# Kernel optimization log

Hardware: AMD Instinct MI355X
Metric: run time of the kernel (lower is better)

Reference implementation:

```python
import jax, jax.numpy as jnp
import numpy as np

NUM_USERS = 100000
NUM_ITEMS = 50000
EMBED = 64
S_NNZ = NUM_USERS * 32   # avg social degree 32
R_NNZ = NUM_USERS * 50   # avg 50 rated items per user
BATCH = 8192


def setup_inputs() -> dict:
    key = jax.random.key(0)
    ks = jax.random.split(key, 12)
    d = EMBED
    # Embedding tables (xavier-uniform style scale)
    U = jax.random.uniform(ks[0], (NUM_USERS, d), jnp.float32, -1.0, 1.0) * np.sqrt(6.0 / (NUM_USERS + d))
    V = jax.random.uniform(ks[1], (NUM_ITEMS, d), jnp.float32, -1.0, 1.0) * np.sqrt(6.0 / (NUM_ITEMS + d))
    # Diffusion layer weights: Linear(2d -> d). Stored as [2d, d] (x @ W + b).
    lim = np.sqrt(6.0 / (3 * d))
    W0 = jax.random.uniform(ks[2], (2 * d, d), jnp.float32, -lim, lim)
    b0 = jnp.zeros((d,), jnp.float32)
    W1 = jax.random.uniform(ks[3], (2 * d, d), jnp.float32, -lim, lim)
    b1 = jnp.zeros((d,), jnp.float32)
    # Sparse social matrix S [NUM_USERS, NUM_USERS], COO edge lists, row-normalized values.
    S_row = jax.random.randint(ks[4], (S_NNZ,), 0, NUM_USERS, jnp.int32)
    S_col = jax.random.randint(ks[5], (S_NNZ,), 0, NUM_USERS, jnp.int32)
    S_val = jnp.full((S_NNZ,), 1.0 / 32.0, jnp.float32)
    # Sparse rating matrix R [NUM_USERS, NUM_ITEMS]
    R_row = jax.random.randint(ks[6], (R_NNZ,), 0, NUM_USERS, jnp.int32)
    R_col = jax.random.randint(ks[7], (R_NNZ,), 0, NUM_ITEMS, jnp.int32)
    R_val = jnp.full((R_NNZ,), 1.0 / 50.0, jnp.float32)
    batch_user = jax.random.randint(ks[8], (BATCH,), 0, NUM_USERS, jnp.int64 if jax.config.jax_enable_x64 else jnp.int32)
    batch_pos_item = jax.random.randint(ks[9], (BATCH,), 0, NUM_ITEMS, jnp.int32)
    batch_neg_item = jax.random.randint(ks[10], (BATCH,), 0, NUM_ITEMS, jnp.int32)
    return dict(batch_user=batch_user, batch_pos_item=batch_pos_item, batch_neg_item=batch_neg_item,
                U=U, V=V, W0=W0, b0=b0, W1=W1, b1=b1,
                S_row=S_row, S_col=S_col, S_val=S_val,
                R_row=R_row, R_col=R_col, R_val=R_val)


def _spmm(row, col, val, X, n_rows):
    # (sparse [n_rows, n] COO) @ X : gather + scale + segment-sum
    return jax.ops.segment_sum(val[:, None] * X[col], row, num_segments=n_rows)


def reference(batch_user, batch_pos_item, batch_neg_item, U, V, W0, b0, W1, b1,
              S_row, S_col, S_val, R_row, R_col, R_val):
    # Diffusion layers: U <- relu(concat([S @ U, U]) @ W + b)
    for W, b in ((W0, b0), (W1, b1)):
        agg = _spmm(S_row, S_col, S_val, U, NUM_USERS)          # [num_users, d]
        U = jax.nn.relu(jnp.concatenate([agg, U], axis=1) @ W + b)
    user_g = U + _spmm(R_row, R_col, R_val, V, NUM_USERS)        # [num_users, d]
    bu = user_g[batch_user]          # [B, d]
    bp = V[batch_pos_item]           # [B, d]
    bn = V[batch_neg_item]           # [B, d]
    return (bu, bp, bn)
```

## Files before the change

kernel.cpp:

```cpp
#include <hip/hip_runtime.h>
#include <hip/hip_bf16.h>

#define NUM_USERS 100000
#define NUM_ITEMS 50000
#define EMBED     64
#define S_NNZ     (NUM_USERS * 32)
#define R_NNZ     (NUM_USERS * 50)
#define BATCH     8192

#define NB    512
#define NCH   1024
#define CHUNK (S_NNZ / NCH)
#define BROWS 196

#define SEGCAP 160


__global__ __launch_bounds__(256) void k_p1hist(const int* __restrict__ rows, int* __restrict__ cnt_t,
                                                int* __restrict__ head, unsigned* __restrict__ bitmap,
                                                int* __restrict__ cntR) {
    __shared__ int h[NB];
    int t = threadIdx.x, b = blockIdx.x;
    int gid = b * 256 + t;
    for (int i = gid; i < NUM_USERS; i += NCH * 256) head[i] = -1;
    for (int i = gid; i < (NUM_USERS + 31) / 32; i += NCH * 256) bitmap[i] = 0;
    for (int i = gid; i < BATCH; i += NCH * 256) cntR[i] = 0;
    for (int i = t; i < NB; i += 256) h[i] = 0;
    __syncthreads();
    int base = b * CHUNK;
    for (int i = t; i < CHUNK; i += 256) atomicAdd(&h[rows[base + i] / BROWS], 1);
    __syncthreads();
    for (int i = t; i < NB; i += 256) cnt_t[i * NCH + b] = h[i];
}

__global__ __launch_bounds__(1024) void k_scan1(const int* __restrict__ cnt, int* __restrict__ excl,
                                                int* __restrict__ bsums, int n,
                                                const int* __restrict__ bu, int* __restrict__ head,
                                                int* __restrict__ nxt, unsigned* __restrict__ bitmap) {
    int t = threadIdx.x;
    int i = blockIdx.x * 1024 + t;
    if (i < BATCH) {
        int u = bu[i];
        nxt[i] = atomicExch(&head[u], i);
        atomicOr(&bitmap[u >> 5], 1u << (u & 31));
    }
    __shared__ int buf[1024];
    int x = (i < n) ? cnt[i] : 0;
    buf[t] = x;
    __syncthreads();
    for (int off = 1; off < 1024; off <<= 1) {
        int y = (t >= off) ? buf[t - off] : 0;
        __syncthreads();
        buf[t] += y;
        __syncthreads();
    }
    if (i < n) excl[i] = buf[t] - x;
    if (t == 1023) bsums[blockIdx.x] = buf[1023];
}

__global__ __launch_bounds__(1024) void k_scan2(int* __restrict__ bsums, int nb, int* __restrict__ total_slot) {
    __shared__ int buf[1024];
    int t = threadIdx.x;
    int x = (t < nb) ? bsums[t] : 0;
    buf[t] = x;
    __syncthreads();
    for (int off = 1; off < 1024; off <<= 1) {
        int y = (t >= off) ? buf[t - off] : 0;
        __syncthreads();
        buf[t] += y;
        __syncthreads();
    }
    if (t < nb) bsums[t] = buf[t] - x;
    if (t == 1023) total_slot[0] = buf[1023];
}

__global__ void k_scan3b(int* __restrict__ a, const int* __restrict__ bsums, int n) {
    int i = blockIdx.x * blockDim.x + threadIdx.x;
    if (i < n) a[i] += bsums[i >> 10];
}

__global__ __launch_bounds__(256) void k_p1scatter(const int* __restrict__ rows, const int* __restrict__ cols,
                                                   const float* __restrict__ vals, const int* __restrict__ cnt_t,
                                                   int2* __restrict__ tmpE,
                                                   const float* __restrict__ U, __hip_bfloat16* __restrict__ U16) {
    __shared__ int cur[NB];
    int t = threadIdx.x, b = blockIdx.x;
    for (int i = t; i < NB; i += 256) cur[i] = cnt_t[i * NCH + b];
    __syncthreads();
    int base = b * CHUNK;
    for (int i = t; i < CHUNK; i += 256) {
        int e  = base + i;
        int r  = rows[e];
        int bk = r / BROWS;
        int pos = atomicAdd(&cur[bk], 1);
        tmpE[pos] = make_int2(((r - bk * BROWS) << 17) | cols[e], __float_as_int(vals[e]));
    }
    const int total = NUM_USERS * EMBED;
    for (int i = b * 256 + t; i < total; i += NCH * 256) U16[i] = __float2bfloat16(U[i]);
}

__global__ __launch_bounds__(512) void k_p2(const int2* __restrict__ tmpE, const int* __restrict__ cnt_t,
                                            int* __restrict__ rowptr, int2* __restrict__ colval) {
    __shared__ int h[512];
    __shared__ int s[512];
    __shared__ int cur[512];
    int t = threadIdx.x, k = blockIdx.x;
    int beg = cnt_t[k * NCH];
    int end = (k < NB - 1) ? cnt_t[(k + 1) * NCH] : S_NNZ;
    h[t] = 0;
    __syncthreads();
    for (int j = beg + t; j < end; j += 512) atomicAdd(&h[((unsigned)tmpE[j].x) >> 17], 1);
    __syncthreads();
    s[t] = h[t];
    __syncthreads();
    for (int off = 1; off < 512; off <<= 1) {
        int y = (t >= off) ? s[t - off] : 0;
        __syncthreads();
        s[t] += y;
        __syncthreads();
    }
    int excl = s[t] - h[t];
    int gr   = k * BROWS + t;
    if (t <= BROWS && gr <= NUM_USERS) rowptr[gr] = beg + excl;
    cur[t] = beg + excl;
    __syncthreads();
    for (int j = beg + t; j < end; j += 512) {
        int2 e  = tmpE[j];
        int pos = atomicAdd(&cur[((unsigned)e.x) >> 17], 1);
        colval[pos] = make_int2(e.x & 0x1FFFF, e.y);
    }
}

__global__ __launch_bounds__(256) void k_spmm16p(const int* __restrict__ rowptr,
                                                 const int2* __restrict__ colval,
                                                 const __hip_bfloat16* __restrict__ X,
                                                 float* __restrict__ Y, int n_pairs) {
    int w    = blockIdx.x * (blockDim.x >> 6) + (threadIdx.x >> 6);
    int lane = threadIdx.x & 63;
    if (w >= n_pairs) return;
    int r0   = 2 * w;
    int beg0 = rowptr[r0], mid = rowptr[r0 + 1], end1 = rowptr[r0 + 2];
    float acc0 = 0.0f, acc1 = 0.0f;
    int j0 = beg0, j1 = mid;
    int jend0 = beg0 + ((mid - beg0) & ~7);
    int jend1 = mid + ((end1 - mid) & ~7);
    while (j0 < jend0 && j1 < jend1) {
        int2 ca[8], cb[8];
#pragma unroll
        for (int u = 0; u < 8; ++u) ca[u] = colval[j0 + u];
#pragma unroll
        for (int u = 0; u < 8; ++u) cb[u] = colval[j1 + u];
        float xa[8], xb[8];
#pragma unroll
        for (int u = 0; u < 8; ++u) xa[u] = __bfloat162float(X[(size_t)ca[u].x * EMBED + lane]);
#pragma unroll
        for (int u = 0; u < 8; ++u) xb[u] = __bfloat162float(X[(size_t)cb[u].x * EMBED + lane]);
#pragma unroll
        for (int u = 0; u < 8; ++u) acc0 = fmaf(__int_as_float(ca[u].y), xa[u], acc0);
#pragma unroll
        for (int u = 0; u < 8; ++u) acc1 = fmaf(__int_as_float(cb[u].y), xb[u], acc1);
        j0 += 8; j1 += 8;
    }
    for (; j0 < jend0; j0 += 8) {
        int2 cv[8];
#pragma unroll
        for (int u = 0; u < 8; ++u) cv[u] = colval[j0 + u];
        float x[8];
#pragma unroll
        for (int u = 0; u < 8; ++u) x[u] = __bfloat162float(X[(size_t)cv[u].x * EMBED + lane]);
#pragma unroll
        for (int u = 0; u < 8; ++u) acc0 = fmaf(__int_as_float(cv[u].y), x[u], acc0);
    }
    for (; j1 < jend1; j1 += 8) {
        int2 cv[8];
#pragma unroll
        for (int u = 0; u < 8; ++u) cv[u] = colval[j1 + u];
        float x[8];
#pragma unroll
        for (int u = 0; u < 8; ++u) x[u] = __bfloat162float(X[(size_t)cv[u].x * EMBED + lane]);
#pragma unroll
        for (int u = 0; u < 8; ++u) acc1 = fmaf(__int_as_float(cv[u].y), x[u], acc1);
    }
    for (; j0 < mid; ++j0)
        acc0 = fmaf(__int_as_float(colval[j0].y), __bfloat162float(X[(size_t)colval[j0].x * EMBED + lane]), acc0);
    for (; j1 < end1; ++j1)
        acc1 = fmaf(__int_as_float(colval[j1].y), __bfloat162float(X[(size_t)colval[j1].x * EMBED + lane]), acc1);
    Y[(size_t)r0 * EMBED + lane]       = acc0;
    Y[(size_t)(r0 + 1) * EMBED + lane] = acc1;
}

__global__ __launch_bounds__(256) void k_spmm_batch16(const int* __restrict__ rowptr,
                                                      const int2* __restrict__ colval,
                                                      const __hip_bfloat16* __restrict__ X,
                                                      const int* __restrict__ bu,
                                                      float* __restrict__ Agg2, int n) {
    int w    = blockIdx.x * (blockDim.x >> 6) + (threadIdx.x >> 6);
    int lane = threadIdx.x & 63;
    if (w >= n) return;
    int r   = bu[w];
    int beg = rowptr[r], end = rowptr[r + 1];
    float acc = 0.0f;
    int j    = beg;
    int jend = beg + ((end - beg) & ~7);
    for (; j < jend; j += 8) {
        int2 cv[8];
#pragma unroll
        for (int u = 0; u < 8; ++u) cv[u] = colval[j + u];
        float x[8];
#pragma unroll
        for (int u = 0; u < 8; ++u) x[u] = __bfloat162float(X[(size_t)cv[u].x * EMBED + lane]);
#pragma unroll
        for (int u = 0; u < 8; ++u) acc = fmaf(__int_as_float(cv[u].y), x[u], acc);
    }
    for (; j < end; ++j)
        acc = fmaf(__int_as_float(colval[j].y), __bfloat162float(X[(size_t)colval[j].x * EMBED + lane]), acc);
    Agg2[(size_t)w * EMBED + lane] = acc;
}


__global__ __launch_bounds__(256) void k_layer(const float* __restrict__ Agg,
                                               const float* __restrict__ Uin,
                                               float* __restrict__ Uout,
                                               __hip_bfloat16* __restrict__ Uout16,
                                               const float* __restrict__ W,
                                               const float* __restrict__ b) {
    __shared__ __align__(16) float Wt[64 * 128];
    int t = threadIdx.x;
    for (int i = t; i < 128 * 64; i += 256) {
        int k = i >> 6, c = i & 63;
        Wt[c * 128 + ((((k >> 2) ^ (c & 7)) << 2) | (k & 3))] = W[i];
    }
    int rl = __builtin_amdgcn_readfirstlane(t >> 6);
    int c  = t & 63;
    int rbase = blockIdx.x * 16 + rl * 4;
    __syncthreads();
    const float4* Wt4 = (const float4*)Wt;
    int  csw   = c & 7;
    int  cbase = c * 32;
    const float4* a0 = (const float4*)(Agg + (size_t)(rbase + 0) * EMBED);
    const float4* a1 = (const float4*)(Agg + (size_t)(rbase + 1) * EMBED);
    const float4* a2 = (const float4*)(Agg + (size_t)(rbase + 2) * EMBED);
    const float4* a3 = (const float4*)(Agg + (size_t)(rbase + 3) * EMBED);
    const float4* u0 = (const float4*)(Uin + (size_t)(rbase + 0) * EMBED);
    const float4* u1 = (const float4*)(Uin + (size_t)(rbase + 1) * EMBED);
    const float4* u2 = (const float4*)(Uin + (size_t)(rbase + 2) * EMBED);
    const float4* u3 = (const float4*)(Uin + (size_t)(rbase + 3) * EMBED);
    float bias = b[c];
    float acc0 = bias, acc1 = bias, acc2 = bias, acc3 = bias;
#pragma unroll 4
    for (int k4 = 0; k4 < 16; ++k4) {
        float4 w4 = Wt4[cbase + (k4 ^ csw)];
        float4 x0 = a0[k4], x1 = a1[k4], x2 = a2[k4], x3 = a3[k4];
        acc0 = fmaf(x0.x, w4.x, acc0); acc0 = fmaf(x0.y, w4.y, acc0); acc0 = fmaf(x0.z, w4.z, acc0); acc0 = fmaf(x0.w, w4.w, acc0);
        acc1 = fmaf(x1.x, w4.x, acc1); acc1 = fmaf(x1.y, w4.y, acc1); acc1 = fmaf(x1.z, w4.z, acc1); acc1 = fmaf(x1.w, w4.w, acc1);
        acc2 = fmaf(x2.x, w4.x, acc2); acc2 = fmaf(x2.y, w4.y, acc2); acc2 = fmaf(x2.z, w4.z, acc2); acc2 = fmaf(x2.w, w4.w, acc2);
        acc3 = fmaf(x3.x, w4.x, acc3); acc3 = fmaf(x3.y, w4.y, acc3); acc3 = fmaf(x3.z, w4.z, acc3); acc3 = fmaf(x3.w, w4.w, acc3);
    }
#pragma unroll 4
    for (int k4 = 16; k4 < 32; ++k4) {
        float4 w4 = Wt4[cbase + (k4 ^ csw)];
        float4 x0 = u0[k4 - 16], x1 = u1[k4 - 16], x2 = u2[k4 - 16], x3 = u3[k4 - 16];
        acc0 = fmaf(x0.x, w4.x, acc0); acc0 = fmaf(x0.y, w4.y, acc0); acc0 = fmaf(x0.z, w4.z, acc0); acc0 = fmaf(x0.w, w4.w, acc0);
        acc1 = fmaf(x1.x, w4.x, acc1); acc1 = fmaf(x1.y, w4.y, acc1); acc1 = fmaf(x1.z, w4.z, acc1); acc1 = fmaf(x1.w, w4.w, acc1);
        acc2 = fmaf(x2.x, w4.x, acc2); acc2 = fmaf(x2.y, w4.y, acc2); acc2 = fmaf(x2.z, w4.z, acc2); acc2 = fmaf(x2.w, w4.w, acc2);
        acc3 = fmaf(x3.x, w4.x, acc3); acc3 = fmaf(x3.y, w4.y, acc3); acc3 = fmaf(x3.z, w4.z, acc3); acc3 = fmaf(x3.w, w4.w, acc3);
    }
    float v0 = fmaxf(acc0, 0.0f), v1 = fmaxf(acc1, 0.0f), v2 = fmaxf(acc2, 0.0f), v3 = fmaxf(acc3, 0.0f);
    Uout[(size_t)(rbase + 0) * EMBED + c] = v0;
    Uout[(size_t)(rbase + 1) * EMBED + c] = v1;
    Uout[(size_t)(rbase + 2) * EMBED + c] = v2;
    Uout[(size_t)(rbase + 3) * EMBED + c] = v3;
    Uout16[(size_t)(rbase + 0) * EMBED + c] = __float2bfloat16(v0);
    Uout16[(size_t)(rbase + 1) * EMBED + c] = __float2bfloat16(v1);
    Uout16[(size_t)(rbase + 2) * EMBED + c] = __float2bfloat16(v2);
    Uout16[(size_t)(rbase + 3) * EMBED + c] = __float2bfloat16(v3);
}

__global__ __launch_bounds__(256) void k_layer_batch(const float* __restrict__ Agg2,
                                                     const float* __restrict__ Uin,
                                                     const int* __restrict__ bu,
                                                     float* __restrict__ out0,
                                                     const float* __restrict__ W,
                                                     const float* __restrict__ b,
                                                     const float* __restrict__ V,
                                                     const int* __restrict__ bp,
                                                     const int* __restrict__ bn) {
    __shared__ __align__(16) float Wt[64 * 128];
    int t = threadIdx.x;
    for (int i = t; i < 128 * 64; i += 256) {
        int k = i >> 6, c = i & 63;
        Wt[c * 128 + ((((k >> 2) ^ (c & 7)) << 2) | (k & 3))] = W[i];
    }
    int rl = __builtin_amdgcn_readfirstlane(t >> 6);
    int c  = t & 63;
    int sbase = blockIdx.x * 16 + rl * 4;
    int r0 = bu[sbase + 0], r1 = bu[sbase + 1], r2 = bu[sbase + 2], r3 = bu[sbase + 3];
    __syncthreads();
    const float4* Wt4 = (const float4*)Wt;
    int  csw   = c & 7;
    int  cbase = c * 32;
    const float4* a0 = (const float4*)(Agg2 + (size_t)(sbase + 0) * EMBED);
    const float4* a1 = (const float4*)(Agg2 + (size_t)(sbase + 1) * EMBED);
    const float4* a2 = (const float4*)(Agg2 + (size_t)(sbase + 2) * EMBED);
    const float4* a3 = (const float4*)(Agg2 + (size_t)(sbase + 3) * EMBED);
    const float4* u0 = (const float4*)(Uin + (size_t)r0 * EMBED);
    const float4* u1 = (const float4*)(Uin + (size_t)r1 * EMBED);
    const float4* u2 = (const float4*)(Uin + (size_t)r2 * EMBED);
    const float4* u3 = (const float4*)(Uin + (size_t)r3 * EMBED);
    float bias = b[c];
    float acc0 = bias, acc1 = bias, acc2 = bias, acc3 = bias;
#pragma unroll 4
    for (int k4 = 0; k4 < 16; ++k4) {
        float4 w4 = Wt4[cbase + (k4 ^ csw)];
        float4 x0 = a0[k4], x1 = a1[k4], x2 = a2[k4], x3 = a3[k4];
        acc0 = fmaf(x0.x, w4.x, acc0); acc0 = fmaf(x0.y, w4.y, acc0); acc0 = fmaf(x0.z, w4.z, acc0); acc0 = fmaf(x0.w, w4.w, acc0);
        acc1 = fmaf(x1.x, w4.x, acc1); acc1 = fmaf(x1.y, w4.y, acc1); acc1 = fmaf(x1.z, w4.z, acc1); acc1 = fmaf(x1.w, w4.w, acc1);
        acc2 = fmaf(x2.x, w4.x, acc2); acc2 = fmaf(x2.y, w4.y, acc2); acc2 = fmaf(x2.z, w4.z, acc2); acc2 = fmaf(x2.w, w4.w, acc2);
        acc3 = fmaf(x3.x, w4.x, acc3); acc3 = fmaf(x3.y, w4.y, acc3); acc3 = fmaf(x3.z, w4.z, acc3); acc3 = fmaf(x3.w, w4.w, acc3);
    }
#pragma unroll 4
    for (int k4 = 16; k4 < 32; ++k4) {
        float4 w4 = Wt4[cbase + (k4 ^ csw)];
        float4 x0 = u0[k4 - 16], x1 = u1[k4 - 16], x2 = u2[k4 - 16], x3 = u3[k4 - 16];
        acc0 = fmaf(x0.x, w4.x, acc0); acc0 = fmaf(x0.y, w4.y, acc0); acc0 = fmaf(x0.z, w4.z, acc0); acc0 = fmaf(x0.w, w4.w, acc0);
        acc1 = fmaf(x1.x, w4.x, acc1); acc1 = fmaf(x1.y, w4.y, acc1); acc1 = fmaf(x1.z, w4.z, acc1); acc1 = fmaf(x1.w, w4.w, acc1);
        acc2 = fmaf(x2.x, w4.x, acc2); acc2 = fmaf(x2.y, w4.y, acc2); acc2 = fmaf(x2.z, w4.z, acc2); acc2 = fmaf(x2.w, w4.w, acc2);
        acc3 = fmaf(x3.x, w4.x, acc3); acc3 = fmaf(x3.y, w4.y, acc3); acc3 = fmaf(x3.z, w4.z, acc3); acc3 = fmaf(x3.w, w4.w, acc3);
    }
    out0[(size_t)(sbase + 0) * EMBED + c] = fmaxf(acc0, 0.0f);
    out0[(size_t)(sbase + 1) * EMBED + c] = fmaxf(acc1, 0.0f);
    out0[(size_t)(sbase + 2) * EMBED + c] = fmaxf(acc2, 0.0f);
    out0[(size_t)(sbase + 3) * EMBED + c] = fmaxf(acc3, 0.0f);
#pragma unroll
    for (int q = 0; q < 4; ++q) {
        int s = sbase + q;
        out0[(size_t)(BATCH + s) * EMBED + c]     = V[(size_t)bp[s] * EMBED + c];
        out0[(size_t)(2 * BATCH + s) * EMBED + c] = V[(size_t)bn[s] * EMBED + c];
    }
}


__global__ __launch_bounds__(256) void k_rseg(const int* __restrict__ rows,
                                              const int* __restrict__ cols,
                                              const float* __restrict__ vals,
                                              const unsigned* __restrict__ bitmap,
                                              const int* __restrict__ head,
                                              int* __restrict__ cntR,
                                              int2* __restrict__ seg, int nnz,
                                              const float* __restrict__ V,
                                              __hip_bfloat16* __restrict__ V16) {
    int e = blockIdx.x * blockDim.x + threadIdx.x;
    if (e < NUM_ITEMS * EMBED) V16[e] = __float2bfloat16(V[e]);
    if (e >= nnz) return;
    int r = rows[e];
    if (!((bitmap[(unsigned)r >> 5] >> (r & 31)) & 1u)) return;
    int s   = head[r];
    int pos = atomicAdd(&cntR[s], 1);
    if (pos < SEGCAP) seg[s * SEGCAP + pos] = make_int2(cols[e], __float_as_int(vals[e]));
}

__global__ __launch_bounds__(256) void k_rspmm(const int* __restrict__ cntR,
                                               const int2* __restrict__ seg,
                                               const __hip_bfloat16* __restrict__ V16,
                                               const int* __restrict__ bu,
                                               const int* __restrict__ head,
                                               const int* __restrict__ nxt,
                                               float* __restrict__ out0) {
    int s    = blockIdx.x * (blockDim.x >> 6) + (threadIdx.x >> 6);
    int lane = threadIdx.x & 63;
    if (s >= BATCH) return;
    if (head[bu[s]] != s) return;
    int n = cntR[s];
    if (n > SEGCAP) n = SEGCAP;
    const int2* cv2 = seg + (size_t)s * SEGCAP;
    float acc = 0.0f;
    int j    = 0;
    int jend = n & ~7;
    for (; j < jend; j += 8) {
        int2 cv[8];
#pragma unroll
        for (int u = 0; u < 8; ++u) cv[u] = cv2[j + u];
        float x[8];
#pragma unroll
        for (int u = 0; u < 8; ++u) x[u] = __bfloat162float(V16[(size_t)cv[u].x * EMBED + lane]);
#pragma unroll
        for (int u = 0; u < 8; ++u) acc = fmaf(__int_as_float(cv[u].y), x[u], acc);
    }
    for (; j < n; ++j)
        acc = fmaf(__int_as_float(cv2[j].y), __bfloat162float(V16[(size_t)cv2[j].x * EMBED + lane]), acc);
    int slot = s;
    while (slot >= 0) {
        out0[(size_t)slot * EMBED + lane] += acc;
        slot = nxt[slot];
    }
}


extern "C" void kernel_launch(void* const* d_in, const int* in_sizes, int n_in,
                              void* d_out, int out_size, void* d_ws, size_t ws_size,
                              hipStream_t stream) {
    const int*   batch_user = (const int*)d_in[0];
    const int*   batch_pos  = (const int*)d_in[1];
    const int*   batch_neg  = (const int*)d_in[2];
    const float* U     = (const float*)d_in[3];
    const float* V     = (const float*)d_in[4];
    const float* W0    = (const float*)d_in[5];
    const float* b0    = (const float*)d_in[6];
    const float* W1    = (const float*)d_in[7];
    const float* b1    = (const float*)d_in[8];
    const int*   S_row = (const int*)d_in[9];
    const int*   S_col = (const int*)d_in[10];
    const float* S_val = (const float*)d_in[11];
    const int*   R_row = (const int*)d_in[12];
    const int*   R_col = (const int*)d_in[13];
    const float* R_val = (const float*)d_in[14];
    float* out = (float*)d_out;

    const size_t tabElems = (size_t)NUM_USERS * EMBED;

    char* wsb = (char*)d_ws;
    size_t o = 0;
    float* A       = (float*)(wsb + o); o += tabElems * 4;
    float* B       = (float*)(wsb + o); o += tabElems * 4;
    float* Agg2    = (float*)(wsb + o); o += (size_t)BATCH * EMBED * 4;
    int*   rowptrS = (int*)(wsb + o);   o += (NUM_USERS + 1) * 4;
    int*   cnt_t   = (int*)(wsb + o);   o += (size_t)NB * NCH * 4;
    int*   bsums   = (int*)(wsb + o);   o += 1024 * 4;
    int*   head    = (int*)(wsb + o);   o += NUM_USERS * 4;
    int*   nxt     = (int*)(wsb + o);   o += BATCH * 4;
    int*   cntR    = (int*)(wsb + o);   o += BATCH * 4;
    unsigned* bitmap = (unsigned*)(wsb + o); o += ((NUM_USERS + 31) / 32) * 4;
    o = (o + 7) & ~(size_t)7;
    int2*  colvalS = (int2*)(wsb + o);  o += (size_t)S_NNZ * 8;
    __hip_bfloat16* X16 = (__hip_bfloat16*)(wsb + o); o += tabElems * 2;

    int2* tmpE = (int2*)A;
    int2* seg  = (int2*)B;

    const int pair_blocks  = (NUM_USERS / 2) / 4;
    const int layer_blocks = (NUM_USERS + 15) / 16;

    k_p1hist<<<NCH, 256, 0, stream>>>(S_row, cnt_t, head, bitmap, cntR);
    k_scan1<<<(NB * NCH) / 1024, 1024, 0, stream>>>(cnt_t, cnt_t, bsums, NB * NCH,
                                                    batch_user, head, nxt, bitmap);
    k_scan2<<<1, 1024, 0, stream>>>(bsums, (NB * NCH) / 1024, &bsums[512]);
    k_scan3b<<<(NB * NCH) / 256, 256, 0, stream>>>(cnt_t, bsums, NB * NCH);
    k_p1scatter<<<NCH, 256, 0, stream>>>(S_row, S_col, S_val, cnt_t, tmpE, U, X16);
    k_p2<<<NB, 512, 0, stream>>>(tmpE, cnt_t, rowptrS, colvalS);

    k_spmm16p<<<pair_blocks, 256, 0, stream>>>(rowptrS, colvalS, X16, B, NUM_USERS / 2);
    k_layer<<<layer_blocks, 256, 0, stream>>>(B, U, A, X16, W0, b0);

    k_spmm_batch16<<<(BATCH * 64 + 255) / 256, 256, 0, stream>>>(rowptrS, colvalS, X16, batch_user, Agg2, BATCH);
    k_layer_batch<<<(BATCH + 15) / 16, 256, 0, stream>>>(Agg2, A, batch_user, out, W1, b1,
                                                         V, batch_pos, batch_neg);

    k_rseg<<<(R_NNZ + 255) / 256, 256, 0, stream>>>(R_row, R_col, R_val, bitmap, head, cntR, seg, R_NNZ,
                                                    V, X16);
    k_rspmm<<<(BATCH * 64 + 255) / 256, 256, 0, stream>>>(cntR, seg, X16, batch_user, head, nxt, out);
}
```

Before: 514.1 us.

## Fuse CSR build pipeline into one cooperative kernel with grid syncs

Six separate launches (histogram, three-stage scan, scatter, per-bucket sort) are merged into one cooperative kernel of 1024 blocks, with grid.sync() between phases. The scan is rewritten so each block covers 512 counts and block 0 scans the 1024 block sums. The aim is to remove launch gaps and the tiny single-block scan kernels. In exchange it pays five grid-wide barriers, and the bucket phase now uses 256 threads per bucket instead of 512, with half the blocks idle.

```diff
diff --git a/kernel.cpp b/kernel.cpp
--- a/kernel.cpp
+++ b/kernel.cpp
@@ -1,5 +1,8 @@
 #include <hip/hip_runtime.h>
 #include <hip/hip_bf16.h>
+#include <hip/hip_cooperative_groups.h>
+
+namespace cg = cooperative_groups;
 
 #define NUM_USERS 100000
 #define NUM_ITEMS 50000
@@ -16,118 +19,132 @@
 #define SEGCAP 160
 
 
-__global__ __launch_bounds__(256) void k_p1hist(const int* __restrict__ rows, int* __restrict__ cnt_t,
-                                                int* __restrict__ head, unsigned* __restrict__ bitmap,
-                                                int* __restrict__ cntR) {
-    __shared__ int h[NB];
+__global__ __launch_bounds__(256) void k_build(const int* __restrict__ rows,
+                                               const int* __restrict__ cols,
+                                               const float* __restrict__ vals,
+                                               int* __restrict__ cnt_t,
+                                               int* __restrict__ head,
+                                               unsigned* __restrict__ bitmap,
+                                               int* __restrict__ cntR,
+                                               const int* __restrict__ bu,
+                                               int* __restrict__ nxt,
+                                               int2* __restrict__ tmpE,
+                                               const float* __restrict__ U,
+                                               __hip_bfloat16* __restrict__ U16,
+                                               int* __restrict__ rowptr,
+                                               int2* __restrict__ colval,
+                                               int* __restrict__ bsums) {
+    cg::grid_group grid = cg::this_grid();
+    __shared__ int sh[768];
     int t = threadIdx.x, b = blockIdx.x;
-    int gid = b * 256 + t;
-    for (int i = gid; i < NUM_USERS; i += NCH * 256) head[i] = -1;
-    for (int i = gid; i < (NUM_USERS + 31) / 32; i += NCH * 256) bitmap[i] = 0;
-    for (int i = gid; i < BATCH; i += NCH * 256) cntR[i] = 0;
-    for (int i = t; i < NB; i += 256) h[i] = 0;
+    int base = b * CHUNK;
+
+    for (int i = b * 256 + t; i < NUM_USERS; i += NCH * 256) head[i] = -1;
+    for (int i = b * 256 + t; i < (NUM_USERS + 31) / 32; i += NCH * 256) bitmap[i] = 0;
+    for (int i = b * 256 + t; i < BATCH; i += NCH * 256) cntR[i] = 0;
+    for (int i = t; i < NB; i += 256) sh[i] = 0;
     __syncthreads();
-    int base = b * CHUNK;
-    for (int i = t; i < CHUNK; i += 256) atomicAdd(&h[rows[base + i] / BROWS], 1);
+    for (int i = t; i < CHUNK; i += 256) atomicAdd(&sh[rows[base + i] / BROWS], 1);
     __syncthreads();
-    for (int i = t; i < NB; i += 256) cnt_t[i * NCH + b] = h[i];
-}
-
-__global__ __launch_bounds__(1024) void k_scan1(const int* __restrict__ cnt, int* __restrict__ excl,
-                                                int* __restrict__ bsums, int n,
-                                                const int* __restrict__ bu, int* __restrict__ head,
-                                                int* __restrict__ nxt, unsigned* __restrict__ bitmap) {
-    int t = threadIdx.x;
-    int i = blockIdx.x * 1024 + t;
-    if (i < BATCH) {
-        int u = bu[i];
-        nxt[i] = atomicExch(&head[u], i);
-        atomicOr(&bitmap[u >> 5], 1u << (u & 31));
-    }
-    __shared__ int buf[1024];
-    int x = (i < n) ? cnt[i] : 0;
-    buf[t] = x;
-    __syncthreads();
-    for (int off = 1; off < 1024; off <<= 1) {
-        int y = (t >= off) ? buf[t - off] : 0;
-        __syncthreads();
-        buf[t] += y;
-        __syncthreads();
-    }
-    if (i < n) excl[i] = buf[t] - x;
-    if (t == 1023) bsums[blockIdx.x] = buf[1023];
-}
-
-__global__ __launch_bounds__(1024) void k_scan2(int* __restrict__ bsums, int nb, int* __restrict__ total_slot) {
-    __shared__ int buf[1024];
-    int t = threadIdx.x;
-    int x = (t < nb) ? bsums[t] : 0;
-    buf[t] = x;
-    __syncthreads();
-    for (int off = 1; off < 1024; off <<= 1) {
-        int y = (t >= off) ? buf[t - off] : 0;
-        __syncthreads();
-        buf[t] += y;
-        __syncthreads();
-    }
-    if (t < nb) bsums[t] = buf[t] - x;
-    if (t == 1023) total_slot[0] = buf[1023];
-}
-
-__global__ void k_scan3b(int* __restrict__ a, const int* __restrict__ bsums, int n) {
-    int i = blockIdx.x * blockDim.x + threadIdx.x;
-    if (i < n) a[i] += bsums[i >> 10];
-}
-
-__global__ __launch_bounds__(256) void k_p1scatter(const int* __restrict__ rows, const int* __restrict__ cols,
-                                                   const float* __restrict__ vals, const int* __restrict__ cnt_t,
-                                                   int2* __restrict__ tmpE,
-                                                   const float* __restrict__ U, __hip_bfloat16* __restrict__ U16) {
-    __shared__ int cur[NB];
-    int t = threadIdx.x, b = blockIdx.x;
-    for (int i = t; i < NB; i += 256) cur[i] = cnt_t[i * NCH + b];
-    __syncthreads();
-    int base = b * CHUNK;
-    for (int i = t; i < CHUNK; i += 256) {
-        int e  = base + i;
-        int r  = rows[e];
-        int bk = r / BROWS;
-        int pos = atomicAdd(&cur[bk], 1);
-        tmpE[pos] = make_int2(((r - bk * BROWS) << 17) | cols[e], __float_as_int(vals[e]));
-    }
-    const int total = NUM_USERS * EMBED;
-    for (int i = b * 256 + t; i < total; i += NCH * 256) U16[i] = __float2bfloat16(U[i]);
-}
-
-__global__ __launch_bounds__(512) void k_p2(const int2* __restrict__ tmpE, const int* __restrict__ cnt_t,
-                                            int* __restrict__ rowptr, int2* __restrict__ colval) {
-    __shared__ int h[512];
-    __shared__ int s[512];
-    __shared__ int cur[512];
-    int t = threadIdx.x, k = blockIdx.x;
-    int beg = cnt_t[k * NCH];
-    int end = (k < NB - 1) ? cnt_t[(k + 1) * NCH] : S_NNZ;
-    h[t] = 0;
-    __syncthreads();
-    for (int j = beg + t; j < end; j += 512) atomicAdd(&h[((unsigned)tmpE[j].x) >> 17], 1);
-    __syncthreads();
-    s[t] = h[t];
-    __syncthreads();
-    for (int off = 1; off < 512; off <<= 1) {
-        int y = (t >= off) ? s[t - off] : 0;
-        __syncthreads();
-        s[t] += y;
-        __syncthreads();
-    }
-    int excl = s[t] - h[t];
-    int gr   = k * BROWS + t;
-    if (t <= BROWS && gr <= NUM_USERS) rowptr[gr] = beg + excl;
-    cur[t] = beg + excl;
-    __syncthreads();
-    for (int j = beg + t; j < end; j += 512) {
-        int2 e  = tmpE[j];
-        int pos = atomicAdd(&cur[((unsigned)e.x) >> 17], 1);
-        colval[pos] = make_int2(e.x & 0x1FFFF, e.y);
+    for (int i = t; i < NB; i += 256) cnt_t[i * NCH + b] = sh[i];
+    grid.sync();
+
+    {
+        int i = b * 256 + t;
+        if (i < BATCH) {
+            int u = bu[i];
+            nxt[i] = atomicExch(&head[u], i);
+            atomicOr(&bitmap[u >> 5], 1u << (u & 31));
+        }
+        int i0 = b * 512 + 2 * t;
+        int x0 = cnt_t[i0], x1 = cnt_t[i0 + 1];
+        int s2 = x0 + x1;
+        sh[t] = s2;
+        __syncthreads();
+        for (int off = 1; off < 256; off <<= 1) {
+            int y = (t >= off) ? sh[t - off] : 0;
+            __syncthreads();
+            sh[t] += y;
+            __syncthreads();
+        }
+        int excl = sh[t] - s2;
+        cnt_t[i0]     = excl;
+        cnt_t[i0 + 1] = excl + x0;
+        if (t == 255) bsums[b] = sh[255];
+    }
+    grid.sync();
+
+    if (b == 0) {
+        int l0 = bsums[4 * t], l1 = bsums[4 * t + 1], l2 = bsums[4 * t + 2], l3 = bsums[4 * t + 3];
+        int s4 = l0 + l1 + l2 + l3;
+        sh[t] = s4;
+        __syncthreads();
+        for (int off = 1; off < 256; off <<= 1) {
+            int y = (t >= off) ? sh[t - off] : 0;
+            __syncthreads();
+            sh[t] += y;
+            __syncthreads();
+        }
+        int excl = sh[t] - s4;
+        bsums[4 * t]     = excl;
+        bsums[4 * t + 1] = excl + l0;
+        bsums[4 * t + 2] = excl + l0 + l1;
+        bsums[4 * t + 3] = excl + l0 + l1 + l2;
+    }
+    grid.sync();
+
+    {
+        int off = bsums[b];
+        int i0  = b * 512 + 2 * t;
+        cnt_t[i0]     += off;
+        cnt_t[i0 + 1] += off;
+    }
+    grid.sync();
+
+    {
+        for (int i = t; i < NB; i += 256) sh[i] = cnt_t[i * NCH + b];
+        __syncthreads();
+        for (int i = t; i < CHUNK; i += 256) {
+            int e  = base + i;
+            int r  = rows[e];
+            int bk = r / BROWS;
+            int pos = atomicAdd(&sh[bk], 1);
+            tmpE[pos] = make_int2(((r - bk * BROWS) << 17) | cols[e], __float_as_int(vals[e]));
+        }
+        const int total = NUM_USERS * EMBED;
+        for (int i = b * 256 + t; i < total; i += NCH * 256) U16[i] = __float2bfloat16(U[i]);
+    }
+    grid.sync();
+
+    if (b < NB) {
+        int k   = b;
+        int beg = cnt_t[k * NCH];
+        int end = (k < NB - 1) ? cnt_t[(k + 1) * NCH] : S_NNZ;
+        int* h2 = sh;
+        int* s2 = sh + 256;
+        int* cu = sh + 512;
+        h2[t] = 0;
+        __syncthreads();
+        for (int j = beg + t; j < end; j += 256) atomicAdd(&h2[((unsigned)tmpE[j].x) >> 17], 1);
+        __syncthreads();
+        s2[t] = h2[t];
+        __syncthreads();
+        for (int off = 1; off < 256; off <<= 1) {
+            int y = (t >= off) ? s2[t - off] : 0;
+            __syncthreads();
+            s2[t] += y;
+            __syncthreads();
+        }
+        int excl = s2[t] - h2[t];
+        int gr   = k * BROWS + t;
+        if (t <= BROWS && gr <= NUM_USERS) rowptr[gr] = beg + excl;
+        cu[t] = beg + excl;
+        __syncthreads();
+        for (int j = beg + t; j < end; j += 256) {
+            int2 e  = tmpE[j];
+            int pos = atomicAdd(&cu[((unsigned)e.x) >> 17], 1);
+            colval[pos] = make_int2(e.x & 0x1FFFF, e.y);
+        }
     }
 }
 
@@ -440,13 +457,13 @@
     const int pair_blocks  = (NUM_USERS / 2) / 4;
     const int layer_blocks = (NUM_USERS + 15) / 16;
 
-    k_p1hist<<<NCH, 256, 0, stream>>>(S_row, cnt_t, head, bitmap, cntR);
-    k_scan1<<<(NB * NCH) / 1024, 1024, 0, stream>>>(cnt_t, cnt_t, bsums, NB * NCH,
-                                                    batch_user, head, nxt, bitmap);
-    k_scan2<<<1, 1024, 0, stream>>>(bsums, (NB * NCH) / 1024, &bsums[512]);
-    k_scan3b<<<(NB * NCH) / 256, 256, 0, stream>>>(cnt_t, bsums, NB * NCH);
-    k_p1scatter<<<NCH, 256, 0, stream>>>(S_row, S_col, S_val, cnt_t, tmpE, U, X16);
-    k_p2<<<NB, 512, 0, stream>>>(tmpE, cnt_t, rowptrS, colvalS);
+    {
+        void* args[] = { (void*)&S_row, (void*)&S_col, (void*)&S_val, (void*)&cnt_t,
+                         (void*)&head, (void*)&bitmap, (void*)&cntR,
+                         (void*)&batch_user, (void*)&nxt, (void*)&tmpE,
+                         (void*)&U, (void*)&X16, (void*)&rowptrS, (void*)&colvalS, (void*)&bsums };
+        hipLaunchCooperativeKernel((const void*)k_build, dim3(NCH), dim3(256), args, 0, stream);
+    }
 
     k_spmm16p<<<pair_blocks, 256, 0, stream>>>(rowptrS, colvalS, X16, B, NUM_USERS / 2);
     k_layer<<<layer_blocks, 256, 0, stream>>>(B, U, A, X16, W0, b0);
```

Measured after the change: 1.081 ms. 110% more time.
